# Optimization experiments

Measured on AMD Instinct MI355X. Metric: run time of the kernel, lower is better.

Reference implementation:

```python
import jax, jax.numpy as jnp
import numpy as np

STALK_DIM = 16
N_NODES = 50000
N_EDGES = 400000
HIDDEN = 64


def setup_inputs() -> dict:
    key = jax.random.key(0)
    k1, k2, k3, k4 = jax.random.split(key, 4)
    d = STALK_DIM
    x = jax.random.normal(k1, (N_NODES, d), dtype=jnp.float32)
    edge_index = jax.random.randint(k2, (2, N_EDGES), 0, N_NODES, dtype=jnp.int64)
    W1 = jax.random.normal(k3, (HIDDEN, 2 * d), dtype=jnp.float32) * (1.0 / np.sqrt(2 * d))
    b1 = jnp.zeros((HIDDEN,), dtype=jnp.float32)
    W2 = jax.random.normal(k4, (d, HIDDEN), dtype=jnp.float32) * (1.0 / np.sqrt(HIDDEN))
    b2 = jnp.zeros((d,), dtype=jnp.float32)
    return {"x": x, "edge_index": edge_index, "W1": W1, "b1": b1, "W2": W2, "b2": b2}


def reference(x, edge_index, W1, b1, W2, b2):
    d = x.shape[1]
    n = x.shape[0]
    src, dst = edge_index[0], edge_index[1]
    xs, xd = x[src], x[dst]  # [E, d]

    def reflection(a, b):
        h = jax.nn.relu(jnp.concatenate([a, b], axis=1) @ W1.T + b1)
        return h @ W2.T + b2  # [E, d]

    def householder(v):
        # F.normalize(v, dim=1): v / max(||v||, 1e-12)
        vn = v / jnp.maximum(jnp.linalg.norm(v, axis=1, keepdims=True), 1e-12)
        return jnp.eye(d, dtype=v.dtype)[None] - 2.0 * vn[:, :, None] * vn[:, None, :]

    F_s = householder(reflection(xs, xd))  # [E, d, d]
    F_d = householder(reflection(xd, xs))  # [E, d, d]
    L_sd = -jnp.einsum('eki,ekj->eij', F_s, F_d)  # -F_s^T @ F_d, [E, d, d]

    # degrees: both endpoints of every edge contribute 1
    ones_e = jnp.ones(src.shape[0], dtype=x.dtype)
    deg = jnp.zeros(n, dtype=x.dtype).at[src].add(ones_e).at[dst].add(ones_e)
    deg_inv_sqrt = 1.0 / jnp.sqrt(jnp.maximum(deg, 1e-5))
    # D_inv_sqrt is scalar*I per node, so normalization is a scalar coefficient per edge
    coef = deg_inv_sqrt[src] * deg_inv_sqrt[dst]  # [E]

    # out[s] -= D^-1/2_s L D^-1/2_d x[d] ; out[d] -= D^-1/2_d L^T D^-1/2_s x[s]
    msg_s = coef[:, None] * jnp.einsum('eij,ej->ei', L_sd, xd)  # goes to src
    msg_d = coef[:, None] * jnp.einsum('eji,ej->ei', L_sd, xs)  # goes to dst

    out = x - jnp.zeros_like(x).at[src].add(msg_s) - jnp.zeros_like(x).at[dst].add(msg_d)
    return jax.nn.relu(out)
```

## Files before the change

kernel.cpp:

```cpp
#include <hip/hip_runtime.h>
#include <hip/hip_bf16.h>

#define N_NODES 50000
#define N_EDGES 400000
#define D 16
#define HID 64

#define SCAN_B 256
#define SCAN_G ((N_NODES + SCAN_B - 1) / SCAN_B)

#define CNT_OFF   0
#define OFF_OFF   (N_NODES)
#define CUR_OFF   (2 * N_NODES + 1)
#define BS_OFF    (3 * N_NODES + 1)
#define BS2_OFF   (BS_OFF + SCAN_B)
#define FLAGS_I   (BS2_OFF + SCAN_B)
#define MSG_OFF   ((FLAGS_I + 2 + 3) & ~3)
#define CSR_NEEDED_BYTES ((size_t)(MSG_OFF + 2 * N_EDGES * D) * 4 + 64)

#define FB_NDEG   (N_NODES)
#define FB_NACC   (N_NODES * D)
#define FB_FLAGS  (FB_NDEG + FB_NACC)

__device__ __forceinline__ float bf_bits(unsigned short us) {
    return __uint_as_float(((unsigned)us) << 16);
}

__device__ __forceinline__ float ld_f(const void* p, int idx, int f32) {
    return f32 ? ((const float*)p)[idx]
               : bf_bits(((const unsigned short*)p)[idx]);
}

__device__ __forceinline__ void load16(const void* __restrict__ p, long long base,
                                       int f32, float* o) {
    if (f32) {
        const float4* q = (const float4*)((const float*)p + base);
        float4 a = q[0], b = q[1], c = q[2], d = q[3];
        o[0]=a.x; o[1]=a.y; o[2]=a.z; o[3]=a.w;
        o[4]=b.x; o[5]=b.y; o[6]=b.z; o[7]=b.w;
        o[8]=c.x; o[9]=c.y; o[10]=c.z; o[11]=c.w;
        o[12]=d.x; o[13]=d.y; o[14]=d.z; o[15]=d.w;
    } else {
        const uint4* q = (const uint4*)((const unsigned short*)p + base);
        uint4 a = q[0], b = q[1];
        unsigned u[8] = {a.x, a.y, a.z, a.w, b.x, b.y, b.z, b.w};
#pragma unroll
        for (int k = 0; k < 8; k++) {
            o[2 * k]     = __uint_as_float(u[k] << 16);
            o[2 * k + 1] = __uint_as_float(u[k] & 0xffff0000u);
        }
    }
}

__device__ __forceinline__ void load_edge(const void* __restrict__ ei, int e, int is64,
                                          int& s, int& d) {
    if (is64) {
        const long long* p = (const long long*)ei;
        s = (int)p[e];
        d = (int)p[N_EDGES + e];
    } else {
        const int* p = (const int*)ei;
        s = p[e];
        d = p[N_EDGES + e];
    }
}

__device__ __forceinline__ void detect_flags(const void* x, const void* ei, int* flags) {
    const unsigned short* h = (const unsigned short*)x;
    int f32 = 0;
    for (int k = 0; k < 256; k++) {
        float v = bf_bits(h[k]);
        if (!(v == v) || fabsf(v) > 1.0e6f) { f32 = 1; break; }
    }
    const long long* p = (const long long*)ei;
    int i64 = 1;
    for (int k = 0; k < 16; k++) {
        long long v = p[k];
        if (v < 0 || v >= N_NODES) { i64 = 0; break; }
    }
    flags[0] = f32;
    flags[1] = i64;
}

__device__ __forceinline__ void edge_math(
    const float* __restrict__ sW1, const float* __restrict__ sW2t,
    const float* __restrict__ sb1, const float* __restrict__ sb2,
    const float* xs, const float* xd, float coef,
    float* ms, float* md)
{
    float vs[D], vd[D];
#pragma unroll
    for (int i = 0; i < D; i++) { vs[i] = sb2[i]; vd[i] = sb2[i]; }

#pragma unroll 4
    for (int j = 0; j < HID; j++) {
        float hs = sb1[j], hd = sb1[j];
        const float* w = &sW1[j * 2 * D];
#pragma unroll
        for (int k = 0; k < D; k++) {
            float w0 = w[k];
            float w1 = w[D + k];
            hs = fmaf(w0, xs[k], hs);
            hs = fmaf(w1, xd[k], hs);
            hd = fmaf(w0, xd[k], hd);
            hd = fmaf(w1, xs[k], hd);
        }
        hs = fmaxf(hs, 0.0f);
        hd = fmaxf(hd, 0.0f);
        const float* w2 = &sW2t[j * D];
#pragma unroll
        for (int i = 0; i < D; i++) {
            vs[i] = fmaf(w2[i], hs, vs[i]);
            vd[i] = fmaf(w2[i], hd, vd[i]);
        }
    }

    float ns = 0.0f, nd = 0.0f;
#pragma unroll
    for (int i = 0; i < D; i++) { ns = fmaf(vs[i], vs[i], ns); nd = fmaf(vd[i], vd[i], nd); }
    float is_ = 1.0f / fmaxf(sqrtf(ns), 1e-12f);
    float id_ = 1.0f / fmaxf(sqrtf(nd), 1e-12f);
#pragma unroll
    for (int i = 0; i < D; i++) { vs[i] *= is_; vd[i] *= id_; }

    float dot1 = 0.0f;
#pragma unroll
    for (int i = 0; i < D; i++) dot1 = fmaf(vd[i], xd[i], dot1);
#pragma unroll
    for (int i = 0; i < D; i++) ms[i] = fmaf(-2.0f * dot1, vd[i], xd[i]);
    float dot2 = 0.0f;
#pragma unroll
    for (int i = 0; i < D; i++) dot2 = fmaf(vs[i], ms[i], dot2);
#pragma unroll
    for (int i = 0; i < D; i++) ms[i] = coef * fmaf(-2.0f * dot2, vs[i], ms[i]);

    float dot3 = 0.0f;
#pragma unroll
    for (int i = 0; i < D; i++) dot3 = fmaf(vs[i], xs[i], dot3);
#pragma unroll
    for (int i = 0; i < D; i++) md[i] = fmaf(-2.0f * dot3, vs[i], xs[i]);
    float dot4 = 0.0f;
#pragma unroll
    for (int i = 0; i < D; i++) dot4 = fmaf(vd[i], md[i], dot4);
#pragma unroll
    for (int i = 0; i < D; i++) md[i] = coef * fmaf(-2.0f * dot4, vd[i], md[i]);
}

__device__ __forceinline__ void stage_weights(
    const void* W1, const void* b1, const void* W2, const void* b2, int f32,
    float* sW1, float* sW2t, float* sb1, float* sb2)
{
    int t = threadIdx.x;
    for (int idx = t; idx < HID * 2 * D; idx += blockDim.x)
        sW1[idx] = ld_f(W1, idx, f32);
    for (int idx = t; idx < HID * D; idx += blockDim.x) {
        int j = idx / D, i = idx % D;
        sW2t[idx] = ld_f(W2, i * HID + j, f32);
    }
    if (t < HID) sb1[t] = ld_f(b1, t, f32);
    if (t < D)  sb2[t] = ld_f(b2, t, f32);
}

__global__ void csr_init_kernel(int* __restrict__ wsI,
                                const void* __restrict__ x,
                                const void* __restrict__ ei) {
    int i = blockIdx.x * blockDim.x + threadIdx.x;
    if (i < N_NODES) wsI[CNT_OFF + i] = 0;
    if (blockIdx.x == 0 && threadIdx.x == 0)
        detect_flags(x, ei, wsI + FLAGS_I);
}

__global__ void csr_count_kernel(const void* __restrict__ ei, int* __restrict__ wsI) {
    int i64 = wsI[FLAGS_I + 1];
    int e = blockIdx.x * blockDim.x + threadIdx.x;
    if (e >= N_EDGES) return;
    int s, d;
    load_edge(ei, e, i64, s, d);
    atomicAdd(&wsI[CNT_OFF + s], 1);
    atomicAdd(&wsI[CNT_OFF + d], 1);
}

__global__ __launch_bounds__(SCAN_B) void csr_scan1_kernel(int* __restrict__ wsI) {
    __shared__ int sm[SCAN_B];
    int t = threadIdx.x;
    int g = blockIdx.x * SCAN_B + t;
    int c = (g < N_NODES) ? wsI[CNT_OFF + g] : 0;
    sm[t] = c;
    __syncthreads();
    for (int st = SCAN_B / 2; st > 0; st >>= 1) {
        if (t < st) sm[t] += sm[t + st];
        __syncthreads();
    }
    if (t == 0) wsI[BS_OFF + blockIdx.x] = sm[0];
}

__global__ __launch_bounds__(SCAN_B) void csr_scan2_kernel(int* __restrict__ wsI) {
    __shared__ int sm[SCAN_B];
    int t = threadIdx.x;
    int v = (t < SCAN_G) ? wsI[BS_OFF + t] : 0;
    sm[t] = v;
    __syncthreads();
    for (int st = 1; st < SCAN_B; st <<= 1) {
        int u = (t >= st) ? sm[t - st] : 0;
        __syncthreads();
        sm[t] += u;
        __syncthreads();
    }
    if (t < SCAN_G) wsI[BS2_OFF + t] = sm[t] - v;
}

__global__ __launch_bounds__(SCAN_B) void csr_scan3_kernel(int* __restrict__ wsI) {
    __shared__ int sm[SCAN_B];
    int t = threadIdx.x;
    int g = blockIdx.x * SCAN_B + t;
    int c = (g < N_NODES) ? wsI[CNT_OFF + g] : 0;
    sm[t] = c;
    __syncthreads();
    for (int st = 1; st < SCAN_B; st <<= 1) {
        int u = (t >= st) ? sm[t - st] : 0;
        __syncthreads();
        sm[t] += u;
        __syncthreads();
    }
    int excl = sm[t] - c + wsI[BS2_OFF + blockIdx.x];
    if (g < N_NODES) {
        wsI[OFF_OFF + g] = excl;
        wsI[CUR_OFF + g] = excl;
        if (g == N_NODES - 1) wsI[OFF_OFF + N_NODES] = excl + c;
    }
}

__global__ __launch_bounds__(256) void csr_edge_kernel(
    const void* __restrict__ x,
    const void* __restrict__ ei,
    const void* __restrict__ W1,
    const void* __restrict__ b1,
    const void* __restrict__ W2,
    const void* __restrict__ b2,
    int* __restrict__ wsI)
{
    __shared__ __align__(16) float sW1[HID * 2 * D];
    __shared__ __align__(16) float sW2t[HID * D];
    __shared__ float sb1[HID];
    __shared__ float sb2[D];

    int f32 = wsI[FLAGS_I];
    int i64 = wsI[FLAGS_I + 1];
    stage_weights(W1, b1, W2, b2, f32, sW1, sW2t, sb1, sb2);
    __syncthreads();

    int e = blockIdx.x * blockDim.x + threadIdx.x;
    if (e >= N_EDGES) return;

    int s, d;
    load_edge(ei, e, i64, s, d);

    float xs[D], xd[D];
    load16(x, (long long)s * D, f32, xs);
    load16(x, (long long)d * D, f32, xd);

    float degs = (float)wsI[CNT_OFF + s];
    float degd = (float)wsI[CNT_OFF + d];
    float coef = (1.0f / sqrtf(fmaxf(degs, 1e-5f))) * (1.0f / sqrtf(fmaxf(degd, 1e-5f)));

    float ms[D], md[D];
    edge_math(sW1, sW2t, sb1, sb2, xs, xd, coef, ms, md);

    float* msg = (float*)(wsI + MSG_OFF);
    int slot_s = atomicAdd(&wsI[CUR_OFF + s], 1);
    float4* m0 = (float4*)(msg + (long long)slot_s * D);
    m0[0] = make_float4(ms[0], ms[1], ms[2], ms[3]);
    m0[1] = make_float4(ms[4], ms[5], ms[6], ms[7]);
    m0[2] = make_float4(ms[8], ms[9], ms[10], ms[11]);
    m0[3] = make_float4(ms[12], ms[13], ms[14], ms[15]);
    int slot_d = atomicAdd(&wsI[CUR_OFF + d], 1);
    float4* m1 = (float4*)(msg + (long long)slot_d * D);
    m1[0] = make_float4(md[0], md[1], md[2], md[3]);
    m1[1] = make_float4(md[4], md[5], md[6], md[7]);
    m1[2] = make_float4(md[8], md[9], md[10], md[11]);
    m1[3] = make_float4(md[12], md[13], md[14], md[15]);
}

__global__ __launch_bounds__(256) void csr_gather_kernel(
    const void* __restrict__ x,
    const int* __restrict__ wsI,
    void* __restrict__ out)
{
    int f32 = wsI[FLAGS_I];
    int n = blockIdx.x * 16 + (threadIdx.x >> 4);
    int i = threadIdx.x & 15;
    if (n >= N_NODES) return;

    const int* off = wsI + OFF_OFF;
    const float* msg = (const float*)(wsI + MSG_OFF);

    int beg = off[n], end = off[n + 1];
    float a = 0.0f;
    for (int it = beg; it < end; it++)
        a += msg[(long long)it * D + i];
    float v = ld_f(x, n * D + i, f32) + a;
    v = fmaxf(v, 0.0f);
    if (f32) ((float*)out)[n * D + i] = v;
    else     ((__hip_bfloat16*)out)[n * D + i] = __float2bfloat16(v);
}

__global__ void fb_init_kernel(float* __restrict__ ws,
                               const void* __restrict__ x,
                               const void* __restrict__ ei) {
    int i = blockIdx.x * blockDim.x + threadIdx.x;
    if (i < FB_FLAGS) ws[i] = 0.0f;
    if (blockIdx.x == 0 && threadIdx.x == 0)
        detect_flags(x, ei, (int*)(ws + FB_FLAGS));
}

__global__ void fb_deg_kernel(const void* __restrict__ ei, float* __restrict__ ws) {
    int i64 = ((const int*)(ws + FB_FLAGS))[1];
    int e = blockIdx.x * blockDim.x + threadIdx.x;
    if (e >= N_EDGES) return;
    int s, d;
    load_edge(ei, e, i64, s, d);
    atomicAdd(&ws[s], 1.0f);
    atomicAdd(&ws[d], 1.0f);
}

__global__ __launch_bounds__(256) void fb_edge_kernel(
    const void* __restrict__ x,
    const void* __restrict__ ei,
    const void* __restrict__ W1,
    const void* __restrict__ b1,
    const void* __restrict__ W2,
    const void* __restrict__ b2,
    float* __restrict__ ws)
{
    __shared__ __align__(16) float sW1[HID * 2 * D];
    __shared__ __align__(16) float sW2t[HID * D];
    __shared__ float sb1[HID];
    __shared__ float sb2[D];

    const int* flags = (const int*)(ws + FB_FLAGS);
    int f32 = flags[0];
    int i64 = flags[1];
    stage_weights(W1, b1, W2, b2, f32, sW1, sW2t, sb1, sb2);
    __syncthreads();

    int e = blockIdx.x * blockDim.x + threadIdx.x;
    if (e >= N_EDGES) return;

    int s, d;
    load_edge(ei, e, i64, s, d);

    float xs[D], xd[D];
    load16(x, (long long)s * D, f32, xs);
    load16(x, (long long)d * D, f32, xd);

    float coef = (1.0f / sqrtf(fmaxf(ws[s], 1e-5f))) * (1.0f / sqrtf(fmaxf(ws[d], 1e-5f)));

    float ms[D], md[D];
    edge_math(sW1, sW2t, sb1, sb2, xs, xd, coef, ms, md);

    float* acc = ws + FB_NDEG;
#pragma unroll
    for (int i = 0; i < D; i++) atomicAdd(&acc[(long long)s * D + i], ms[i]);
#pragma unroll
    for (int i = 0; i < D; i++) atomicAdd(&acc[(long long)d * D + i], md[i]);
}

__global__ void fb_finalize_kernel(const void* __restrict__ x,
                                   const float* __restrict__ ws,
                                   void* __restrict__ out)
{
    int f32 = ((const int*)(ws + FB_FLAGS))[0];
    const float* acc = ws + FB_NDEG;
    int i = blockIdx.x * blockDim.x + threadIdx.x;
    if (i >= FB_NACC) return;
    float v = ld_f(x, i, f32) + acc[i];
    v = fmaxf(v, 0.0f);
    if (f32) ((float*)out)[i] = v;
    else     ((__hip_bfloat16*)out)[i] = __float2bfloat16(v);
}

extern "C" void kernel_launch(void* const* d_in, const int* in_sizes, int n_in,
                              void* d_out, int out_size, void* d_ws, size_t ws_size,
                              hipStream_t stream)
{
    const void* x  = d_in[0];
    const void* ei = d_in[1];
    const void* W1 = d_in[2];
    const void* b1 = d_in[3];
    const void* W2 = d_in[4];
    const void* b2 = d_in[5];

    int blk = 256;
    if (ws_size >= CSR_NEEDED_BYTES) {
        int* wsI = (int*)d_ws;
        csr_init_kernel<<<(N_NODES + blk - 1) / blk, blk, 0, stream>>>(wsI, x, ei);
        csr_count_kernel<<<(N_EDGES + blk - 1) / blk, blk, 0, stream>>>(ei, wsI);
        csr_scan1_kernel<<<SCAN_G, SCAN_B, 0, stream>>>(wsI);
        csr_scan2_kernel<<<1, SCAN_B, 0, stream>>>(wsI);
        csr_scan3_kernel<<<SCAN_G, SCAN_B, 0, stream>>>(wsI);
        csr_edge_kernel<<<(N_EDGES + blk - 1) / blk, blk, 0, stream>>>(x, ei, W1, b1, W2, b2, wsI);
        csr_gather_kernel<<<(N_NODES + 15) / 16, blk, 0, stream>>>(x, wsI, d_out);
    } else {
        float* ws = (float*)d_ws;
        fb_init_kernel<<<(FB_FLAGS + blk - 1) / blk, blk, 0, stream>>>(ws, x, ei);
        fb_deg_kernel<<<(N_EDGES + blk - 1) / blk, blk, 0, stream>>>(ei, ws);
        fb_edge_kernel<<<(N_EDGES + blk - 1) / blk, blk, 0, stream>>>(x, ei, W1, b1, W2, b2, ws);
        fb_finalize_kernel<<<(FB_NACC + blk - 1) / blk, blk, 0, stream>>>(x, ws, d_out);
    }
}
```

Before: 209.7 us.

## Compute edge MLP with bf16 MFMA and restructure CSR degree counting

Replaces the per-thread scalar FP32 edge MLP with a persistent-grid kernel. Each wave computes 16 edge-directions through bf16 MFMA 16x16x32 for both layers, with weights held in registers and hidden activations staged in LDS. The Householder reflections become 16-lane shuffle reductions. Degree counting is split across four replicated counters to reduce atomic contention, and the separate block-scan kernel is folded into scan3. Running x and the activations in bf16 adds rounding error relative to the FP32 reference, and the new kernel adds more syncthreads per iteration.

```diff
diff --git a/kernel.cpp b/kernel.cpp
--- a/kernel.cpp
+++ b/kernel.cpp
@@ -8,27 +8,39 @@
 
 #define SCAN_B 256
 #define SCAN_G ((N_NODES + SCAN_B - 1) / SCAN_B)
-
-#define CNT_OFF   0
-#define OFF_OFF   (N_NODES)
-#define CUR_OFF   (2 * N_NODES + 1)
-#define BS_OFF    (3 * N_NODES + 1)
-#define BS2_OFF   (BS_OFF + SCAN_B)
-#define FLAGS_I   (BS2_OFF + SCAN_B)
-#define MSG_OFF   ((FLAGS_I + 2 + 3) & ~3)
-#define CSR_NEEDED_BYTES ((size_t)(MSG_OFF + 2 * N_EDGES * D) * 4 + 64)
+#define EPB 32
+
+typedef __attribute__((ext_vector_type(8))) short bf16x8;
+typedef __attribute__((ext_vector_type(4))) float f32x4;
+typedef unsigned short ushort_t;
+
+#define CNT4_OFF  0
+#define DEG_OFF   (4 * N_NODES)
+#define OFF_OFF   (5 * N_NODES)
+#define CUR_OFF   (6 * N_NODES + 1)
+#define BS_OFF    (7 * N_NODES + 1)
+#define FLAGS_I   (BS_OFF + SCAN_G)
+#define MSG_OFF_I (((FLAGS_I + 2) + 3) & ~3)
+#define CSR_NEEDED_BYTES ((size_t)(MSG_OFF_I + 2 * N_EDGES * D) * 4 + 64)
 
 #define FB_NDEG   (N_NODES)
 #define FB_NACC   (N_NODES * D)
 #define FB_FLAGS  (FB_NDEG + FB_NACC)
 
-__device__ __forceinline__ float bf_bits(unsigned short us) {
+__device__ __forceinline__ float bf_bits(ushort_t us) {
     return __uint_as_float(((unsigned)us) << 16);
 }
-
+__device__ __forceinline__ ushort_t f2bf(float v) {
+    unsigned u = __float_as_uint(v);
+    unsigned r = (u + 0x7fffu + ((u >> 16) & 1u)) >> 16;
+    return (ushort_t)r;
+}
 __device__ __forceinline__ float ld_f(const void* p, int idx, int f32) {
     return f32 ? ((const float*)p)[idx]
-               : bf_bits(((const unsigned short*)p)[idx]);
+               : bf_bits(((const ushort_t*)p)[idx]);
+}
+__device__ __forceinline__ ushort_t ld_bf_bits(const void* p, int idx, int f32) {
+    return f32 ? f2bf(((const float*)p)[idx]) : ((const ushort_t*)p)[idx];
 }
 
 __device__ __forceinline__ void load16(const void* __restrict__ p, long long base,
@@ -41,7 +53,7 @@
         o[8]=c.x; o[9]=c.y; o[10]=c.z; o[11]=c.w;
         o[12]=d.x; o[13]=d.y; o[14]=d.z; o[15]=d.w;
     } else {
-        const uint4* q = (const uint4*)((const unsigned short*)p + base);
+        const uint4* q = (const uint4*)((const ushort_t*)p + base);
         uint4 a = q[0], b = q[1];
         unsigned u[8] = {a.x, a.y, a.z, a.w, b.x, b.y, b.z, b.w};
 #pragma unroll
@@ -49,6 +61,19 @@
             o[2 * k]     = __uint_as_float(u[k] << 16);
             o[2 * k + 1] = __uint_as_float(u[k] & 0xffff0000u);
         }
+    }
+}
+
+__device__ __forceinline__ void load_row_bf16(const void* __restrict__ x, long long node,
+                                              int f32, uint4& a, uint4& b) {
+    if (!f32) {
+        const uint4* p = (const uint4*)((const ushort_t*)x + node * D);
+        a = p[0]; b = p[1];
+    } else {
+        union { ushort_t u[16]; uint4 q[2]; } t;
+#pragma unroll
+        for (int k = 0; k < 16; k++) t.u[k] = f2bf(((const float*)x)[node * D + k]);
+        a = t.q[0]; b = t.q[1];
     }
 }
 
@@ -66,7 +91,7 @@
 }
 
 __device__ __forceinline__ void detect_flags(const void* x, const void* ei, int* flags) {
-    const unsigned short* h = (const unsigned short*)x;
+    const ushort_t* h = (const ushort_t*)x;
     int f32 = 0;
     for (int k = 0; k < 256; k++) {
         float v = bf_bits(h[k]);
@@ -82,90 +107,19 @@
     flags[1] = i64;
 }
 
-__device__ __forceinline__ void edge_math(
-    const float* __restrict__ sW1, const float* __restrict__ sW2t,
-    const float* __restrict__ sb1, const float* __restrict__ sb2,
-    const float* xs, const float* xd, float coef,
-    float* ms, float* md)
-{
-    float vs[D], vd[D];
-#pragma unroll
-    for (int i = 0; i < D; i++) { vs[i] = sb2[i]; vd[i] = sb2[i]; }
-
-#pragma unroll 4
-    for (int j = 0; j < HID; j++) {
-        float hs = sb1[j], hd = sb1[j];
-        const float* w = &sW1[j * 2 * D];
-#pragma unroll
-        for (int k = 0; k < D; k++) {
-            float w0 = w[k];
-            float w1 = w[D + k];
-            hs = fmaf(w0, xs[k], hs);
-            hs = fmaf(w1, xd[k], hs);
-            hd = fmaf(w0, xd[k], hd);
-            hd = fmaf(w1, xs[k], hd);
-        }
-        hs = fmaxf(hs, 0.0f);
-        hd = fmaxf(hd, 0.0f);
-        const float* w2 = &sW2t[j * D];
-#pragma unroll
-        for (int i = 0; i < D; i++) {
-            vs[i] = fmaf(w2[i], hs, vs[i]);
-            vd[i] = fmaf(w2[i], hd, vd[i]);
-        }
-    }
-
-    float ns = 0.0f, nd = 0.0f;
-#pragma unroll
-    for (int i = 0; i < D; i++) { ns = fmaf(vs[i], vs[i], ns); nd = fmaf(vd[i], vd[i], nd); }
-    float is_ = 1.0f / fmaxf(sqrtf(ns), 1e-12f);
-    float id_ = 1.0f / fmaxf(sqrtf(nd), 1e-12f);
-#pragma unroll
-    for (int i = 0; i < D; i++) { vs[i] *= is_; vd[i] *= id_; }
-
-    float dot1 = 0.0f;
-#pragma unroll
-    for (int i = 0; i < D; i++) dot1 = fmaf(vd[i], xd[i], dot1);
-#pragma unroll
-    for (int i = 0; i < D; i++) ms[i] = fmaf(-2.0f * dot1, vd[i], xd[i]);
-    float dot2 = 0.0f;
-#pragma unroll
-    for (int i = 0; i < D; i++) dot2 = fmaf(vs[i], ms[i], dot2);
-#pragma unroll
-    for (int i = 0; i < D; i++) ms[i] = coef * fmaf(-2.0f * dot2, vs[i], ms[i]);
-
-    float dot3 = 0.0f;
-#pragma unroll
-    for (int i = 0; i < D; i++) dot3 = fmaf(vs[i], xs[i], dot3);
-#pragma unroll
-    for (int i = 0; i < D; i++) md[i] = fmaf(-2.0f * dot3, vs[i], xs[i]);
-    float dot4 = 0.0f;
-#pragma unroll
-    for (int i = 0; i < D; i++) dot4 = fmaf(vd[i], md[i], dot4);
-#pragma unroll
-    for (int i = 0; i < D; i++) md[i] = coef * fmaf(-2.0f * dot4, vd[i], md[i]);
-}
-
-__device__ __forceinline__ void stage_weights(
-    const void* W1, const void* b1, const void* W2, const void* b2, int f32,
-    float* sW1, float* sW2t, float* sb1, float* sb2)
-{
-    int t = threadIdx.x;
-    for (int idx = t; idx < HID * 2 * D; idx += blockDim.x)
-        sW1[idx] = ld_f(W1, idx, f32);
-    for (int idx = t; idx < HID * D; idx += blockDim.x) {
-        int j = idx / D, i = idx % D;
-        sW2t[idx] = ld_f(W2, i * HID + j, f32);
-    }
-    if (t < HID) sb1[t] = ld_f(b1, t, f32);
-    if (t < D)  sb2[t] = ld_f(b2, t, f32);
+__device__ __forceinline__ float red16(float v) {
+    v += __shfl_xor(v, 1);
+    v += __shfl_xor(v, 2);
+    v += __shfl_xor(v, 4);
+    v += __shfl_xor(v, 8);
+    return v;
 }
 
 __global__ void csr_init_kernel(int* __restrict__ wsI,
                                 const void* __restrict__ x,
                                 const void* __restrict__ ei) {
     int i = blockIdx.x * blockDim.x + threadIdx.x;
-    if (i < N_NODES) wsI[CNT_OFF + i] = 0;
+    if (i < 4 * N_NODES) wsI[CNT4_OFF + i] = 0;
     if (blockIdx.x == 0 && threadIdx.x == 0)
         detect_flags(x, ei, wsI + FLAGS_I);
 }
@@ -176,15 +130,21 @@
     if (e >= N_EDGES) return;
     int s, d;
     load_edge(ei, e, i64, s, d);
-    atomicAdd(&wsI[CNT_OFF + s], 1);
-    atomicAdd(&wsI[CNT_OFF + d], 1);
+    int r = (e & 3) * N_NODES;
+    atomicAdd(&wsI[CNT4_OFF + r + s], 1);
+    atomicAdd(&wsI[CNT4_OFF + r + d], 1);
 }
 
 __global__ __launch_bounds__(SCAN_B) void csr_scan1_kernel(int* __restrict__ wsI) {
     __shared__ int sm[SCAN_B];
     int t = threadIdx.x;
     int g = blockIdx.x * SCAN_B + t;
-    int c = (g < N_NODES) ? wsI[CNT_OFF + g] : 0;
+    int c = 0;
+    if (g < N_NODES) {
+        c = wsI[CNT4_OFF + g] + wsI[CNT4_OFF + N_NODES + g]
+          + wsI[CNT4_OFF + 2 * N_NODES + g] + wsI[CNT4_OFF + 3 * N_NODES + g];
+        wsI[DEG_OFF + g] = c;
+    }
     sm[t] = c;
     __syncthreads();
     for (int st = SCAN_B / 2; st > 0; st >>= 1) {
@@ -194,26 +154,23 @@
     if (t == 0) wsI[BS_OFF + blockIdx.x] = sm[0];
 }
 
-__global__ __launch_bounds__(SCAN_B) void csr_scan2_kernel(int* __restrict__ wsI) {
+__global__ __launch_bounds__(SCAN_B) void csr_scan3_kernel(int* __restrict__ wsI) {
+    __shared__ int sB[SCAN_B];
     __shared__ int sm[SCAN_B];
     int t = threadIdx.x;
-    int v = (t < SCAN_G) ? wsI[BS_OFF + t] : 0;
-    sm[t] = v;
+    int bsv = (t < SCAN_G) ? wsI[BS_OFF + t] : 0;
+    sB[t] = bsv;
     __syncthreads();
     for (int st = 1; st < SCAN_B; st <<= 1) {
-        int u = (t >= st) ? sm[t - st] : 0;
-        __syncthreads();
-        sm[t] += u;
-        __syncthreads();
-    }
-    if (t < SCAN_G) wsI[BS2_OFF + t] = sm[t] - v;
-}
-
-__global__ __launch_bounds__(SCAN_B) void csr_scan3_kernel(int* __restrict__ wsI) {
-    __shared__ int sm[SCAN_B];
-    int t = threadIdx.x;
+        int u = (t >= st) ? sB[t - st] : 0;
+        __syncthreads();
+        sB[t] += u;
+        __syncthreads();
+    }
+    int blockBase = sB[blockIdx.x] - wsI[BS_OFF + blockIdx.x];
+
     int g = blockIdx.x * SCAN_B + t;
-    int c = (g < N_NODES) ? wsI[CNT_OFF + g] : 0;
+    int c = (g < N_NODES) ? wsI[DEG_OFF + g] : 0;
     sm[t] = c;
     __syncthreads();
     for (int st = 1; st < SCAN_B; st <<= 1) {
@@ -222,7 +179,7 @@
         sm[t] += u;
         __syncthreads();
     }
-    int excl = sm[t] - c + wsI[BS2_OFF + blockIdx.x];
+    int excl = sm[t] - c + blockBase;
     if (g < N_NODES) {
         wsI[OFF_OFF + g] = excl;
         wsI[CUR_OFF + g] = excl;
@@ -230,7 +187,10 @@
     }
 }
 
-__global__ __launch_bounds__(256) void csr_edge_kernel(
+#define SA_STRIDE 40
+#define SH_STRIDE 80
+
+__global__ __launch_bounds__(256) void csr_edge_mfma_kernel(
     const void* __restrict__ x,
     const void* __restrict__ ei,
     const void* __restrict__ W1,
@@ -239,46 +199,137 @@
     const void* __restrict__ b2,
     int* __restrict__ wsI)
 {
-    __shared__ __align__(16) float sW1[HID * 2 * D];
-    __shared__ __align__(16) float sW2t[HID * D];
-    __shared__ float sb1[HID];
-    __shared__ float sb2[D];
-
-    int f32 = wsI[FLAGS_I];
-    int i64 = wsI[FLAGS_I + 1];
-    stage_weights(W1, b1, W2, b2, f32, sW1, sW2t, sb1, sb2);
-    __syncthreads();
-
-    int e = blockIdx.x * blockDim.x + threadIdx.x;
-    if (e >= N_EDGES) return;
-
-    int s, d;
-    load_edge(ei, e, i64, s, d);
-
-    float xs[D], xd[D];
-    load16(x, (long long)s * D, f32, xs);
-    load16(x, (long long)d * D, f32, xd);
-
-    float degs = (float)wsI[CNT_OFF + s];
-    float degd = (float)wsI[CNT_OFF + d];
-    float coef = (1.0f / sqrtf(fmaxf(degs, 1e-5f))) * (1.0f / sqrtf(fmaxf(degd, 1e-5f)));
-
-    float ms[D], md[D];
-    edge_math(sW1, sW2t, sb1, sb2, xs, xd, coef, ms, md);
-
-    float* msg = (float*)(wsI + MSG_OFF);
-    int slot_s = atomicAdd(&wsI[CUR_OFF + s], 1);
-    float4* m0 = (float4*)(msg + (long long)slot_s * D);
-    m0[0] = make_float4(ms[0], ms[1], ms[2], ms[3]);
-    m0[1] = make_float4(ms[4], ms[5], ms[6], ms[7]);
-    m0[2] = make_float4(ms[8], ms[9], ms[10], ms[11]);
-    m0[3] = make_float4(ms[12], ms[13], ms[14], ms[15]);
-    int slot_d = atomicAdd(&wsI[CUR_OFF + d], 1);
-    float4* m1 = (float4*)(msg + (long long)slot_d * D);
-    m1[0] = make_float4(md[0], md[1], md[2], md[3]);
-    m1[1] = make_float4(md[4], md[5], md[6], md[7]);
-    m1[2] = make_float4(md[8], md[9], md[10], md[11]);
-    m1[3] = make_float4(md[12], md[13], md[14], md[15]);
+    __shared__ __align__(16) short sA[64 * SA_STRIDE];
+    __shared__ __align__(16) short sH[4][16 * SH_STRIDE];
+    __shared__ int   sSlot[64];
+    __shared__ float sCoef[32];
+
+    const int f32 = wsI[FLAGS_I];
+    const int i64 = wsI[FLAGS_I + 1];
+    float* msg = (float*)(wsI + MSG_OFF_I);
+
+    const int tid = threadIdx.x;
+    const int w  = tid >> 6;
+    const int lm = tid & 63;
+    const int m  = lm & 15;
+    const int q  = lm >> 4;
+
+    bf16x8 b1f[4];
+#pragma unroll
+    for (int nt = 0; nt < 4; nt++)
+#pragma unroll
+        for (int j = 0; j < 8; j++)
+            b1f[nt][j] = (short)ld_bf_bits(W1, (16 * nt + m) * 32 + 8 * q + j, f32);
+    bf16x8 b2f[2];
+#pragma unroll
+    for (int kt = 0; kt < 2; kt++)
+#pragma unroll
+        for (int j = 0; j < 8; j++)
+            b2f[kt][j] = (short)ld_bf_bits(W2, m * 64 + 32 * kt + 8 * q + j, f32);
+    float bias1v[4];
+#pragma unroll
+    for (int nt = 0; nt < 4; nt++) bias1v[nt] = ld_f(b1, 16 * nt + m, f32);
+    const float bias2v = ld_f(b2, m, f32);
+
+    for (long long base = (long long)blockIdx.x * EPB; base < N_EDGES;
+         base += (long long)gridDim.x * EPB) {
+        __syncthreads();
+
+        {
+            int i = tid >> 3;
+            int r = tid & 7;
+            int e = (int)base + i;
+            if (r < 4) {
+                int s, d;
+                load_edge(ei, e, i64, s, d);
+                if (r == 0) {
+                    uint4 a, b;
+                    load_row_bf16(x, s, f32, a, b);
+                    *(uint4*)&sA[(2 * i) * SA_STRIDE]          = a;
+                    *(uint4*)&sA[(2 * i) * SA_STRIDE + 8]      = b;
+                    *(uint4*)&sA[(2 * i + 1) * SA_STRIDE + 16] = a;
+                    *(uint4*)&sA[(2 * i + 1) * SA_STRIDE + 24] = b;
+                } else if (r == 1) {
+                    uint4 a, b;
+                    load_row_bf16(x, d, f32, a, b);
+                    *(uint4*)&sA[(2 * i) * SA_STRIDE + 16]     = a;
+                    *(uint4*)&sA[(2 * i) * SA_STRIDE + 24]     = b;
+                    *(uint4*)&sA[(2 * i + 1) * SA_STRIDE]      = a;
+                    *(uint4*)&sA[(2 * i + 1) * SA_STRIDE + 8]  = b;
+                } else if (r == 2) {
+                    sSlot[2 * i] = atomicAdd(&wsI[CUR_OFF + s], 1);
+                    float degs = (float)wsI[DEG_OFF + s];
+                    float degd = (float)wsI[DEG_OFF + d];
+                    sCoef[i] = (1.0f / sqrtf(fmaxf(degs, 1e-5f)))
+                             * (1.0f / sqrtf(fmaxf(degd, 1e-5f)));
+                } else {
+                    sSlot[2 * i + 1] = atomicAdd(&wsI[CUR_OFF + d], 1);
+                }
+            }
+        }
+        __syncthreads();
+
+        bf16x8 a1 = *(const bf16x8*)&sA[(16 * w + m) * SA_STRIDE + q * 8];
+        f32x4 z4 = {0.0f, 0.0f, 0.0f, 0.0f};
+        f32x4 hacc[4];
+#pragma unroll
+        for (int nt = 0; nt < 4; nt++)
+            hacc[nt] = __builtin_amdgcn_mfma_f32_16x16x32_bf16(a1, b1f[nt], z4, 0, 0, 0);
+
+#pragma unroll
+        for (int nt = 0; nt < 4; nt++)
+#pragma unroll
+            for (int r = 0; r < 4; r++) {
+                float hv = fmaxf(hacc[nt][r] + bias1v[nt], 0.0f);
+                sH[w][(4 * q + r) * SH_STRIDE + 16 * nt + m] = (short)f2bf(hv);
+            }
+        __syncthreads();
+
+        bf16x8 a20 = *(const bf16x8*)&sH[w][m * SH_STRIDE + q * 8];
+        bf16x8 a21 = *(const bf16x8*)&sH[w][m * SH_STRIDE + 32 + q * 8];
+        f32x4 vacc = __builtin_amdgcn_mfma_f32_16x16x32_bf16(a20, b2f[0], z4, 0, 0, 0);
+        vacc = __builtin_amdgcn_mfma_f32_16x16x32_bf16(a21, b2f[1], vacc, 0, 0, 0);
+
+        float vn[4];
+#pragma unroll
+        for (int r = 0; r < 4; r++) {
+            float v = vacc[r] + bias2v;
+            float nsq = red16(v * v);
+            vn[r] = v * (1.0f / fmaxf(sqrtf(nsq), 1e-12f));
+        }
+        int rowA = 16 * w + 4 * q;
+        float xsA = bf_bits((ushort_t)sA[rowA * SA_STRIDE + m]);
+        float xdA = bf_bits((ushort_t)sA[rowA * SA_STRIDE + 16 + m]);
+        float xsB = bf_bits((ushort_t)sA[(rowA + 2) * SA_STRIDE + m]);
+        float xdB = bf_bits((ushort_t)sA[(rowA + 2) * SA_STRIDE + 16 + m]);
+        int iA = 8 * w + 2 * q;
+        float cA = sCoef[iA], cB = sCoef[iA + 1];
+
+        {
+            float d1 = red16(vn[1] * xdA);
+            float t  = fmaf(-2.0f * d1, vn[1], xdA);
+            float d2 = red16(vn[0] * t);
+            float ms = cA * fmaf(-2.0f * d2, vn[0], t);
+            float d3 = red16(vn[0] * xsA);
+            float u  = fmaf(-2.0f * d3, vn[0], xsA);
+            float d4 = red16(vn[1] * u);
+            float md = cA * fmaf(-2.0f * d4, vn[1], u);
+            msg[(long long)sSlot[2 * iA] * D + m]     = ms;
+            msg[(long long)sSlot[2 * iA + 1] * D + m] = md;
+        }
+        {
+            float d1 = red16(vn[3] * xdB);
+            float t  = fmaf(-2.0f * d1, vn[3], xdB);
+            float d2 = red16(vn[2] * t);
+            float ms = cB * fmaf(-2.0f * d2, vn[2], t);
+            float d3 = red16(vn[2] * xsB);
+            float u  = fmaf(-2.0f * d3, vn[2], xsB);
+            float d4 = red16(vn[3] * u);
+            float md = cB * fmaf(-2.0f * d4, vn[3], u);
+            msg[(long long)sSlot[2 * iA + 2] * D + m] = ms;
+            msg[(long long)sSlot[2 * iA + 3] * D + m] = md;
+        }
+    }
 }
 
 __global__ __launch_bounds__(256) void csr_gather_kernel(
@@ -292,7 +343,7 @@
     if (n >= N_NODES) return;
 
     const int* off = wsI + OFF_OFF;
-    const float* msg = (const float*)(wsI + MSG_OFF);
+    const float* msg = (const float*)(wsI + MSG_OFF_I);
 
     int beg = off[n], end = off[n + 1];
     float a = 0.0f;
@@ -304,6 +355,80 @@
     else     ((__hip_bfloat16*)out)[n * D + i] = __float2bfloat16(v);
 }
 
+__device__ __forceinline__ void edge_math(
+    const float* __restrict__ sW1, const float* __restrict__ sW2t,
+    const float* __restrict__ sb1, const float* __restrict__ sb2,
+    const float* xs, const float* xd, float coef,
+    float* ms, float* md)
+{
+    float vs[D], vd[D];
+#pragma unroll
+    for (int i = 0; i < D; i++) { vs[i] = sb2[i]; vd[i] = sb2[i]; }
+#pragma unroll 4
+    for (int j = 0; j < HID; j++) {
+        float hs = sb1[j], hd = sb1[j];
+        const float* w = &sW1[j * 2 * D];
+#pragma unroll
+        for (int k = 0; k < D; k++) {
+            float w0 = w[k], w1 = w[D + k];
+            hs = fmaf(w0, xs[k], hs);
+            hs = fmaf(w1, xd[k], hs);
+            hd = fmaf(w0, xd[k], hd);
+            hd = fmaf(w1, xs[k], hd);
+        }
+        hs = fmaxf(hs, 0.0f);
+        hd = fmaxf(hd, 0.0f);
+        const float* w2 = &sW2t[j * D];
+#pragma unroll
+        for (int i = 0; i < D; i++) {
+            vs[i] = fmaf(w2[i], hs, vs[i]);
+            vd[i] = fmaf(w2[i], hd, vd[i]);
+        }
+    }
+    float ns = 0.0f, nd = 0.0f;
+#pragma unroll
+    for (int i = 0; i < D; i++) { ns = fmaf(vs[i], vs[i], ns); nd = fmaf(vd[i], vd[i], nd); }
+    float is_ = 1.0f / fmaxf(sqrtf(ns), 1e-12f);
+    float id_ = 1.0f / fmaxf(sqrtf(nd), 1e-12f);
+#pragma unroll
+    for (int i = 0; i < D; i++) { vs[i] *= is_; vd[i] *= id_; }
+    float dot1 = 0.0f;
+#pragma unroll
+    for (int i = 0; i < D; i++) dot1 = fmaf(vd[i], xd[i], dot1);
+#pragma unroll
+    for (int i = 0; i < D; i++) ms[i] = fmaf(-2.0f * dot1, vd[i], xd[i]);
+    float dot2 = 0.0f;
+#pragma unroll
+    for (int i = 0; i < D; i++) dot2 = fmaf(vs[i], ms[i], dot2);
+#pragma unroll
+    for (int i = 0; i < D; i++) ms[i] = coef * fmaf(-2.0f * dot2, vs[i], ms[i]);
+    float dot3 = 0.0f;
+#pragma unroll
+    for (int i = 0; i < D; i++) dot3 = fmaf(vs[i], xs[i], dot3);
+#pragma unroll
+    for (int i = 0; i < D; i++) md[i] = fmaf(-2.0f * dot3, vs[i], xs[i]);
+    float dot4 = 0.0f;
+#pragma unroll
+    for (int i = 0; i < D; i++) dot4 = fmaf(vd[i], md[i], dot4);
+#pragma unroll
+    for (int i = 0; i < D; i++) md[i] = coef * fmaf(-2.0f * dot4, vd[i], md[i]);
+}
+
+__device__ __forceinline__ void stage_weights(
+    const void* W1, const void* b1, const void* W2, const void* b2, int f32,
+    float* sW1, float* sW2t, float* sb1, float* sb2)
+{
+    int t = threadIdx.x;
+    for (int idx = t; idx < HID * 2 * D; idx += blockDim.x)
+        sW1[idx] = ld_f(W1, idx, f32);
+    for (int idx = t; idx < HID * D; idx += blockDim.x) {
+        int j = idx / D, i = idx % D;
+        sW2t[idx] = ld_f(W2, i * HID + j, f32);
+    }
+    if (t < HID) sb1[t] = ld_f(b1, t, f32);
+    if (t < D)  sb2[t] = ld_f(b2, t, f32);
+}
+
 __global__ void fb_init_kernel(float* __restrict__ ws,
                                const void* __restrict__ x,
                                const void* __restrict__ ei) {
@@ -324,40 +449,29 @@
 }
 
 __global__ __launch_bounds__(256) void fb_edge_kernel(
-    const void* __restrict__ x,
-    const void* __restrict__ ei,
-    const void* __restrict__ W1,
-    const void* __restrict__ b1,
-    const void* __restrict__ W2,
-    const void* __restrict__ b2,
+    const void* __restrict__ x, const void* __restrict__ ei,
+    const void* __restrict__ W1, const void* __restrict__ b1,
+    const void* __restrict__ W2, const void* __restrict__ b2,
     float* __restrict__ ws)
 {
     __shared__ __align__(16) float sW1[HID * 2 * D];
     __shared__ __align__(16) float sW2t[HID * D];
     __shared__ float sb1[HID];
     __shared__ float sb2[D];
-
     const int* flags = (const int*)(ws + FB_FLAGS);
-    int f32 = flags[0];
-    int i64 = flags[1];
+    int f32 = flags[0], i64 = flags[1];
     stage_weights(W1, b1, W2, b2, f32, sW1, sW2t, sb1, sb2);
     __syncthreads();
-
     int e = blockIdx.x * blockDim.x + threadIdx.x;
     if (e >= N_EDGES) return;
-
     int s, d;
     load_edge(ei, e, i64, s, d);
-
     float xs[D], xd[D];
     load16(x, (long long)s * D, f32, xs);
     load16(x, (long long)d * D, f32, xd);
-
     float coef = (1.0f / sqrtf(fmaxf(ws[s], 1e-5f))) * (1.0f / sqrtf(fmaxf(ws[d], 1e-5f)));
-
     float ms[D], md[D];
     edge_math(sW1, sW2t, sb1, sb2, xs, xd, coef, ms, md);
-
     float* acc = ws + FB_NDEG;
 #pragma unroll
     for (int i = 0; i < D; i++) atomicAdd(&acc[(long long)s * D + i], ms[i]);
@@ -393,12 +507,11 @@
     int blk = 256;
     if (ws_size >= CSR_NEEDED_BYTES) {
         int* wsI = (int*)d_ws;
-        csr_init_kernel<<<(N_NODES + blk - 1) / blk, blk, 0, stream>>>(wsI, x, ei);
+        csr_init_kernel<<<(4 * N_NODES + blk - 1) / blk, blk, 0, stream>>>(wsI, x, ei);
         csr_count_kernel<<<(N_EDGES + blk - 1) / blk, blk, 0, stream>>>(ei, wsI);
         csr_scan1_kernel<<<SCAN_G, SCAN_B, 0, stream>>>(wsI);
-        csr_scan2_kernel<<<1, SCAN_B, 0, stream>>>(wsI);
         csr_scan3_kernel<<<SCAN_G, SCAN_B, 0, stream>>>(wsI);
-        csr_edge_kernel<<<(N_EDGES + blk - 1) / blk, blk, 0, stream>>>(x, ei, W1, b1, W2, b2, wsI);
+        csr_edge_mfma_kernel<<<2048, blk, 0, stream>>>(x, ei, W1, b1, W2, b2, wsI);
         csr_gather_kernel<<<(N_NODES + 15) / 16, blk, 0, stream>>>(x, wsI, d_out);
     } else {
         float* ws = (float*)d_ws;
```

Result: slower. 240.6 us (+14.8%).
